# Kernel optimization log

Hardware: AMD Instinct MI355X
Metric: run time of the kernel (lower is better)

## Reference

```python
import jax, jax.numpy as jnp
import numpy as np

B, C, H, W = 8, 16, 128, 128
P = H * W            # pixel_number = 16384
KN = 16              # kernel_number_per_pixel
CK = C * 9           # in_channel * kernel_size = 144


def setup_inputs() -> dict:
    key = jax.random.key(0)
    k1, k2, k3 = jax.random.split(key, 3)
    x = jax.random.normal(k1, (B, C, H, W), dtype=jnp.float32)
    weights = jax.random.normal(k2, (P, KN, CK), dtype=jnp.float32)
    hash_idx = jax.random.randint(k3, (P, CK), 0, C * H * W, dtype=jnp.int64)
    return {"x": x, "weights": weights, "hash_idx": hash_idx}


def reference(x, weights, hash_idx):
    b, c, h, w = x.shape
    img_size = c * h * w
    flat = x.reshape(-1)  # [B*C*H*W]
    # per-batch offset of the per-pixel hash table (torch fallback branch)
    idx = hash_idx[None, :, :] + (jnp.arange(b, dtype=hash_idx.dtype) * img_size)[:, None, None]  # [B,P,CK]
    patches = flat[idx]  # [B, P, CK] hash-indexed gather (im2col)
    # weights [P,KN,CK] @ patches [P,CK,B] -> [P,KN,B]; transpose(0,2) -> [B,KN,P]
    return jnp.einsum('pkc,bpc->bkp', weights, patches)
```

## Files before the change

### kernel.cpp

```cpp
#include <hip/hip_runtime.h>
#include <hip/hip_bf16.h>

#define P_TOTAL 16384
#define KN      16
#define CK      144
#define BATCH   8
#define IMG     262144
#define PATCH_H 160

typedef __attribute__((ext_vector_type(8))) short bf16x8;
typedef __attribute__((ext_vector_type(4))) float f32x4;

__device__ __forceinline__ short f2bf(float f) {
    __hip_bfloat16 h = __float2bfloat16(f);
    return *reinterpret_cast<short*>(&h);
}

__global__ __launch_bounds__(256) void transpose_x_bf16(
    const float* __restrict__ x, float4* __restrict__ xt)
{
    const int i = blockIdx.x * 256 + threadIdx.x;
    union { short h[8]; float4 f4; } u;
#pragma unroll
    for (int b = 0; b < BATCH; ++b)
        u.h[b] = f2bf(x[(size_t)b * IMG + i]);
    xt[i] = u.f4;
}

__global__ __launch_bounds__(256) void gather_patches(
    const float4* __restrict__ xt,
    const int*    __restrict__ hidx,
    unsigned short* __restrict__ patches)
{
    const int t    = threadIdx.x;
    const int wv   = t >> 6;
    const int lane = t & 63;
    const int bid  = blockIdx.x;
    const int p    = (bid & 7) * (P_TOTAL / 8) + (bid >> 3) * 4 + wv;

    const int* hp = hidx + p * CK;
    unsigned short* pp = patches + (size_t)p * BATCH * PATCH_H;

    union { unsigned short h[8]; float4 f4; } u0, u1, u2;
    u0.f4 = xt[hp[lane]];
    u1.f4 = xt[hp[lane + 64]];
    const bool tail = lane < (CK - 128);
    if (tail) u2.f4 = xt[hp[lane + 128]];

#pragma unroll
    for (int b = 0; b < BATCH; ++b) pp[b * PATCH_H + lane]       = u0.h[b];
#pragma unroll
    for (int b = 0; b < BATCH; ++b) pp[b * PATCH_H + lane + 64]  = u1.h[b];
    if (tail) {
#pragma unroll
        for (int b = 0; b < BATCH; ++b) pp[b * PATCH_H + lane + 128] = u2.h[b];
    } else if (lane < 32) {
#pragma unroll
        for (int b = 0; b < BATCH; ++b) pp[b * PATCH_H + lane + 128] = 0;
    }
}

__global__ __launch_bounds__(256) void gemm_mfma(
    const unsigned short* __restrict__ patches,
    const float* __restrict__ w,
    float* __restrict__ out)
{
    const int t    = threadIdx.x;
    const int wv   = t >> 6;
    const int lane = t & 63;
    const int bid  = blockIdx.x;
    const int p    = (bid & 7) * (P_TOTAL / 8) + (bid >> 3) * 4 + wv;

    const int n    = lane & 15;
    const int q    = lane >> 4;
    const int arow = n & 7;
    const unsigned short* ap = patches + (size_t)p * BATCH * PATCH_H + (size_t)arow * PATCH_H;
    const float* wp = w + (size_t)p * (KN * CK) + (size_t)n * CK;

    f32x4 acc = {0.f, 0.f, 0.f, 0.f};
#pragma unroll
    for (int s = 0; s < 5; ++s) {
        const int c = 32 * s + 8 * q;
        bf16x8 a = *reinterpret_cast<const bf16x8*>(ap + c);
        bf16x8 b = {0, 0, 0, 0, 0, 0, 0, 0};
        if (c < CK) {
            const float4 f0 = *reinterpret_cast<const float4*>(wp + c);
            const float4 f1 = *reinterpret_cast<const float4*>(wp + c + 4);
            b[0] = f2bf(f0.x); b[1] = f2bf(f0.y); b[2] = f2bf(f0.z); b[3] = f2bf(f0.w);
            b[4] = f2bf(f1.x); b[5] = f2bf(f1.y); b[6] = f2bf(f1.z); b[7] = f2bf(f1.w);
        }
        acc = __builtin_amdgcn_mfma_f32_16x16x32_bf16(a, b, acc, 0, 0, 0);
    }

    if (lane < 32) {
#pragma unroll
        for (int i = 0; i < 4; ++i) {
            const int b = q * 4 + i;
            out[(size_t)b * (KN * P_TOTAL) + (size_t)n * P_TOTAL + p] = acc[i];
        }
    }
}

__global__ __launch_bounds__(256) void abc2d_fallback(
    const float* __restrict__ x, const float* __restrict__ w,
    const int* __restrict__ hidx, float* __restrict__ out)
{
    __shared__ float patch[CK * 12];
    const int bid = blockIdx.x;
    const int p   = (bid & 7) * (P_TOTAL / 8) + (bid >> 3);
    const int t   = threadIdx.x;
    const int* hp = hidx + p * CK;
    for (int j = t; j < CK * BATCH; j += 256) {
        const int c = j >> 3, b = j & 7;
        patch[c * 12 + b] = x[(size_t)hp[c] + (size_t)b * IMG];
    }
    __syncthreads();
    const int k = t >> 4, cs = t & 15;
    const float* wp = w + (size_t)p * (KN * CK) + (size_t)k * CK;
    float acc[BATCH];
#pragma unroll
    for (int b = 0; b < BATCH; ++b) acc[b] = 0.f;
#pragma unroll
    for (int i = 0; i < 9; ++i) {
        const int c = cs + 16 * i;
        const float wv = wp[c];
        const float* pr = &patch[c * 12];
#pragma unroll
        for (int b = 0; b < BATCH; ++b) acc[b] += wv * pr[b];
    }
#pragma unroll
    for (int b = 0; b < BATCH; ++b) {
        float v = acc[b];
        v += __shfl_xor(v, 1); v += __shfl_xor(v, 2);
        v += __shfl_xor(v, 4); v += __shfl_xor(v, 8);
        acc[b] = v;
    }
    if (cs == 0)
#pragma unroll
        for (int b = 0; b < BATCH; ++b)
            out[(size_t)b * (KN * P_TOTAL) + (size_t)k * P_TOTAL + p] = acc[b];
}

extern "C" void kernel_launch(void* const* d_in, const int* in_sizes, int n_in,
                              void* d_out, int out_size, void* d_ws, size_t ws_size,
                              hipStream_t stream) {
    const float* x    = (const float*)d_in[0];
    const float* wts  = (const float*)d_in[1];
    const int*   hidx = (const int*)d_in[2];
    float* out = (float*)d_out;

    const size_t xt_bytes    = (size_t)IMG * BATCH * sizeof(short);
    const size_t patch_bytes = (size_t)P_TOTAL * BATCH * PATCH_H * sizeof(short);
    const size_t patch_off   = 8u << 20;

    if (ws_size >= patch_off + patch_bytes) {
        float4* xt = (float4*)d_ws;
        unsigned short* patches = (unsigned short*)((char*)d_ws + patch_off);
        transpose_x_bf16<<<IMG / 256, 256, 0, stream>>>(x, xt);
        gather_patches<<<P_TOTAL / 4, 256, 0, stream>>>(xt, hidx, patches);
        gemm_mfma<<<P_TOTAL / 4, 256, 0, stream>>>(patches, wts, out);
    } else {
        abc2d_fallback<<<P_TOTAL, 256, 0, stream>>>(x, wts, hidx, out);
    }
}
```

Baseline: 256.9 us.

## Split patch gather into two passes by source-index half for cache locality

The random gather from the transposed bf16 image is split into two kernel launches. Each launch only fetches indices that fall in one half of the source table, so each pass touches a 2 MB working set that fits better in cache. In exchange the index table is read twice and one extra launch is added, and each pass diverges on a data-dependent branch.

New measurement: 271.3 us. 1.06x slower.

```diff
diff --git a/kernel.cpp b/kernel.cpp
--- a/kernel.cpp
+++ b/kernel.cpp
@@ -27,9 +27,10 @@
     xt[i] = u.f4;
 }
 
-__global__ __launch_bounds__(256) void gather_patches(
-    const float4* __restrict__ xt,
-    const int*    __restrict__ hidx,
+template <int PASS>
+__global__ __launch_bounds__(256) void gather_half(
+    const float4*   __restrict__ xt,
+    const int*      __restrict__ hidx,
     unsigned short* __restrict__ patches)
 {
     const int t    = threadIdx.x;
@@ -38,23 +39,34 @@
     const int bid  = blockIdx.x;
     const int p    = (bid & 7) * (P_TOTAL / 8) + (bid >> 3) * 4 + wv;
 
+    const int LO = PASS ? (IMG / 2) : 0;
+    const int HI = PASS ? IMG : (IMG / 2);
+
     const int* hp = hidx + p * CK;
     unsigned short* pp = patches + (size_t)p * BATCH * PATCH_H;
 
-    union { unsigned short h[8]; float4 f4; } u0, u1, u2;
-    u0.f4 = xt[hp[lane]];
-    u1.f4 = xt[hp[lane + 64]];
     const bool tail = lane < (CK - 128);
-    if (tail) u2.f4 = xt[hp[lane + 128]];
+    const int id0 = hp[lane];
+    const int id1 = hp[lane + 64];
+    const int id2 = tail ? hp[lane + 128] : 0;
 
+    union { unsigned short h[8]; float4 f4; } u;
+    if (id0 >= LO && id0 < HI) {
+        u.f4 = xt[id0];
 #pragma unroll
-    for (int b = 0; b < BATCH; ++b) pp[b * PATCH_H + lane]       = u0.h[b];
+        for (int b = 0; b < BATCH; ++b) pp[b * PATCH_H + lane] = u.h[b];
+    }
+    if (id1 >= LO && id1 < HI) {
+        u.f4 = xt[id1];
 #pragma unroll
-    for (int b = 0; b < BATCH; ++b) pp[b * PATCH_H + lane + 64]  = u1.h[b];
-    if (tail) {
+        for (int b = 0; b < BATCH; ++b) pp[b * PATCH_H + lane + 64] = u.h[b];
+    }
+    if (tail && id2 >= LO && id2 < HI) {
+        u.f4 = xt[id2];
 #pragma unroll
-        for (int b = 0; b < BATCH; ++b) pp[b * PATCH_H + lane + 128] = u2.h[b];
-    } else if (lane < 32) {
+        for (int b = 0; b < BATCH; ++b) pp[b * PATCH_H + lane + 128] = u.h[b];
+    }
+    if (PASS == 0 && !tail && lane < 32) {
 #pragma unroll
         for (int b = 0; b < BATCH; ++b) pp[b * PATCH_H + lane + 128] = 0;
     }
@@ -149,7 +161,6 @@
     const int*   hidx = (const int*)d_in[2];
     float* out = (float*)d_out;
 
-    const size_t xt_bytes    = (size_t)IMG * BATCH * sizeof(short);
     const size_t patch_bytes = (size_t)P_TOTAL * BATCH * PATCH_H * sizeof(short);
     const size_t patch_off   = 8u << 20;
 
@@ -157,7 +168,8 @@
         float4* xt = (float4*)d_ws;
         unsigned short* patches = (unsigned short*)((char*)d_ws + patch_off);
         transpose_x_bf16<<<IMG / 256, 256, 0, stream>>>(x, xt);
-        gather_patches<<<P_TOTAL / 4, 256, 0, stream>>>(xt, hidx, patches);
+        gather_half<0><<<P_TOTAL / 4, 256, 0, stream>>>(xt, hidx, patches);
+        gather_half<1><<<P_TOTAL / 4, 256, 0, stream>>>(xt, hidx, patches);
         gemm_mfma<<<P_TOTAL / 4, 256, 0, stream>>>(patches, wts, out);
     } else {
         abc2d_fallback<<<P_TOTAL, 256, 0, stream>>>(x, wts, hidx, out);
```
